# Kernel optimization log

Measured on AMD Instinct MI355X. Metric: run time of the kernel, lower is better.

Reference implementation:

```python
import jax, jax.numpy as jnp
import numpy as np

D_MODEL = 512
EPS = 1e-5


def setup_inputs() -> dict:
    key = jax.random.key(0)
    k1, k2, k3 = jax.random.split(key, 3)
    B, N, D = 8, 2048, D_MODEL
    output = jax.random.normal(k1, (B, N, D), dtype=jnp.float32)
    # multiplicative 0/1 float mask over the [B, N, N] score matrix
    slf_attn_mask = jax.random.randint(k2, (B, N, N), 0, 2).astype(jnp.float32)
    # nn.Linear(d_model, d_model): weight [out, in], xavier-uniform; bias zeros-ish
    limit = float(np.sqrt(6.0 / (D + D)))
    W = jax.random.uniform(k3, (D, D), dtype=jnp.float32, minval=-limit, maxval=limit)
    b = jnp.zeros((D,), dtype=jnp.float32)
    return {"output": output, "slf_attn_mask": slf_attn_mask, "W": W, "b": b}


def reference(output, slf_attn_mask, W, b):
    temperature = jnp.asarray(D_MODEL, output.dtype) ** 0.5
    # scores: [B, N, N] = (q / temp) @ k^T, then multiplicative mask
    attn = jnp.einsum("bnd,bmd->bnm", output / temperature, output) * slf_attn_mask
    # F.normalize(p=2, dim=-1, eps=1e-5): x / max(||x||_2, eps)
    norm = jnp.sqrt(jnp.sum(attn * attn, axis=-1, keepdims=True))
    attn = attn / jnp.maximum(norm, EPS)
    # values: elu(Linear(output)), Linear uses W @ x + b with W [out, in]
    v = jax.nn.elu(jnp.einsum("bnd,ed->bne", output, W) + b)
    return jnp.einsum("bnm,bme->bne", attn, v)
```

## Files before the change

kernel.cpp:

```cpp
#include <hip/hip_runtime.h>
#include <hip/hip_bf16.h>

#define NSEQ 2048
#define DM 512
#define BATCH 8
#define GTOT (BATCH * NSEQ)
#define INV_T 0.044194173824159216f
#define EPSN 1e-5f

typedef __bf16 bf16_t;
typedef bf16_t bf16x8 __attribute__((ext_vector_type(8)));
typedef float f32x16 __attribute__((ext_vector_type(16)));
typedef unsigned short u16;
typedef unsigned int u32;
typedef unsigned long long u64;

__device__ __forceinline__ u16 f2bf(float f) {
    u32 u = __builtin_bit_cast(u32, f);
    u32 r = (u + 0x7FFFu + ((u >> 16) & 1u)) >> 16;
    return (u16)r;
}

__device__ __forceinline__ void async16(const u16* g, u16* l) {
    __builtin_amdgcn_global_load_lds(
        (const __attribute__((address_space(1))) u32*)g,
        (__attribute__((address_space(3))) u32*)l, 16, 0, 0);
}

__device__ __forceinline__ bf16x8 fragld64(const u16* t, int row, int kc) {
    return *(const bf16x8*)(t + row * 64 + ((kc ^ ((row >> 1) & 7)) << 3));
}

#define MFMA32(a, b, c) __builtin_amdgcn_mfma_f32_32x32x16_bf16(a, b, c, 0, 0, 0)
#define ROWOFF(reg, lh) (((reg) & 3) + 8 * ((reg) >> 2) + 4 * (lh))

#define STAGE64(Ag, ldA, Bg, ldB, k0)                                            \
    do {                                                                         \
        _Pragma("unroll") for (int j = 0; j < 4; ++j) {                          \
            const int cg = (lane & 7) ^ ((j * 4 + (lane >> 4)) & 7);             \
            const int dst = (wave * 4 + j) * 512 + lane * 8;                     \
            async16((Ag) + (long)(rS + j * 8) * (ldA) + (k0) + cg * 8, Ab + dst);\
            async16((Bg) + (long)(rS + j * 8) * (ldB) + (k0) + cg * 8, Bb + dst);\
        }                                                                        \
    } while (0)

__global__ __launch_bounds__(256) void k_convert(
    const float* __restrict__ X, const float* __restrict__ W,
    u16* __restrict__ Kbf, u16* __restrict__ Wbf, float* __restrict__ ssbuf) {
    const long NK = (long)GTOT * DM / 4;
    const long NW = (long)DM * DM / 4;
    const long NS = GTOT / 4;
    long i = (long)blockIdx.x * 256 + threadIdx.x;
    if (i < NK) {
        float4 f = ((const float4*)X)[i];
        ushort4 o;
        o.x = f2bf(f.x); o.y = f2bf(f.y); o.z = f2bf(f.z); o.w = f2bf(f.w);
        ((ushort4*)Kbf)[i] = o;
    } else if (i < NK + NW) {
        long j = i - NK;
        float4 f = ((const float4*)W)[j];
        ushort4 o;
        o.x = f2bf(f.x); o.y = f2bf(f.y); o.z = f2bf(f.z); o.w = f2bf(f.w);
        ((ushort4*)Wbf)[j] = o;
    } else if (i < NK + NW + NS) {
        ((float4*)ssbuf)[i - NK - NW] = (float4){0.f, 0.f, 0.f, 0.f};
    }
}

__global__ __launch_bounds__(256, 4) void k_sgemm(
    const u16* __restrict__ Kbf, const float* __restrict__ mask,
    u16* __restrict__ Sbuf, float* __restrict__ ssbuf) {
    __shared__ __attribute__((aligned(16))) u16 Ab[8192], Bb[8192];
    const int tid = threadIdx.x, wave = tid >> 6, lane = tid & 63;
    const int l31 = lane & 31, lh = lane >> 5;
    const int wy = wave >> 1, wx = wave & 1;
    const int bid = blockIdx.x;
    const int b = bid & 7;
    const int ty = (bid >> 3) & 15, tx = bid >> 7;
    const int M0 = ty * 128, N0 = tx * 128;
    const u16* Ag = Kbf + (long)(b * NSEQ + M0) * DM;
    const u16* Bg = Kbf + (long)(b * NSEQ + N0) * DM;

    const int rS = wave * 32 + (lane >> 3);

    f32x16 acc[2][2];
#pragma unroll
    for (int i = 0; i < 2; ++i)
#pragma unroll
        for (int j = 0; j < 2; ++j)
#pragma unroll
            for (int e = 0; e < 16; ++e) acc[i][j][e] = 0.f;

    for (int kt = 0; kt < 8; ++kt) {
        const int k0 = kt * 64;
        __syncthreads();
        STAGE64(Ag, DM, Bg, DM, k0);
        __syncthreads();
#pragma unroll
        for (int ks = 0; ks < 4; ++ks) {
            const int kc = ks * 2 + lh;
            bf16x8 a0 = fragld64(Ab, wy * 64 + l31, kc);
            bf16x8 a1 = fragld64(Ab, wy * 64 + 32 + l31, kc);
            bf16x8 b0 = fragld64(Bb, wx * 64 + l31, kc);
            bf16x8 b1 = fragld64(Bb, wx * 64 + 32 + l31, kc);
            acc[0][0] = MFMA32(a0, b0, acc[0][0]);
            acc[0][1] = MFMA32(a0, b1, acc[0][1]);
            acc[1][0] = MFMA32(a1, b0, acc[1][0]);
            acc[1][1] = MFMA32(a1, b1, acc[1][1]);
        }
    }
#pragma unroll
    for (int mi = 0; mi < 2; ++mi) {
#pragma unroll
        for (int reg = 0; reg < 16; ++reg) {
            int rl = M0 + wy * 64 + mi * 32 + ROWOFF(reg, lh);
            long rg = (long)b * NSEQ + rl;
            const float* mrow = mask + rg * NSEQ;
            float v = 0.f;
#pragma unroll
            for (int ni = 0; ni < 2; ++ni) {
                int cg = N0 + wx * 64 + ni * 32 + l31;
                float s = acc[mi][ni][reg] * INV_T * mrow[cg];
                v += s * s;
                Sbuf[rg * NSEQ + cg] = f2bf(s);
            }
            v += __shfl_xor(v, 1, 32);
            v += __shfl_xor(v, 2, 32);
            v += __shfl_xor(v, 4, 32);
            v += __shfl_xor(v, 8, 32);
            v += __shfl_xor(v, 16, 32);
            if (l31 == 0) atomicAdd(&ssbuf[rg], v);
        }
    }
}

__global__ __launch_bounds__(256, 4) void k_vgemm(
    const u16* __restrict__ Wbf, const u16* __restrict__ Kbf,
    const float* __restrict__ bias, u16* __restrict__ vT) {
    __shared__ __attribute__((aligned(16))) u16 Ab[8192], Bb[8192];
    const int tid = threadIdx.x, wave = tid >> 6, lane = tid & 63;
    const int l31 = lane & 31, lh = lane >> 5;
    const int wy = wave >> 1, wx = wave & 1;
    const int M0 = blockIdx.y * 128, N0 = blockIdx.x * 128;
    const u16* Ag = Wbf + (long)M0 * DM;
    const u16* Bg = Kbf + (long)N0 * DM;

    const int rS = wave * 32 + (lane >> 3);

    f32x16 acc[2][2];
#pragma unroll
    for (int i = 0; i < 2; ++i)
#pragma unroll
        for (int j = 0; j < 2; ++j)
#pragma unroll
            for (int e = 0; e < 16; ++e) acc[i][j][e] = 0.f;

    for (int kt = 0; kt < 8; ++kt) {
        const int k0 = kt * 64;
        __syncthreads();
        STAGE64(Ag, DM, Bg, DM, k0);
        __syncthreads();
#pragma unroll
        for (int ks = 0; ks < 4; ++ks) {
            const int kc = ks * 2 + lh;
            bf16x8 a0 = fragld64(Ab, wy * 64 + l31, kc);
            bf16x8 a1 = fragld64(Ab, wy * 64 + 32 + l31, kc);
            bf16x8 b0 = fragld64(Bb, wx * 64 + l31, kc);
            bf16x8 b1 = fragld64(Bb, wx * 64 + 32 + l31, kc);
            acc[0][0] = MFMA32(a0, b0, acc[0][0]);
            acc[0][1] = MFMA32(a0, b1, acc[0][1]);
            acc[1][0] = MFMA32(a1, b0, acc[1][0]);
            acc[1][1] = MFMA32(a1, b1, acc[1][1]);
        }
    }
#pragma unroll
    for (int mi = 0; mi < 2; ++mi) {
#pragma unroll
        for (int reg = 0; reg < 16; ++reg) {
            int e = M0 + wy * 64 + mi * 32 + ROWOFF(reg, lh);
            float bv = bias[e];
#pragma unroll
            for (int ni = 0; ni < 2; ++ni) {
                int g = N0 + wx * 64 + ni * 32 + l31;
                float x = acc[mi][ni][reg] + bv;
                float v = x > 0.f ? x : (__expf(x) - 1.f);
                vT[(long)e * GTOT + g] = f2bf(v);
            }
        }
    }
}

__global__ __launch_bounds__(256, 4) void k_pv(
    const u16* __restrict__ Sbuf, const u16* __restrict__ vT,
    const float* __restrict__ ssbuf, float* __restrict__ Out) {
    __shared__ __attribute__((aligned(16))) u16 Ab[8192], Bb[8192];
    __shared__ float sc[128];
    const int tid = threadIdx.x, wave = tid >> 6, lane = tid & 63;
    const int l31 = lane & 31, lh = lane >> 5;
    const int wy = wave >> 1, wx = wave & 1;
    const int bid = blockIdx.x;
    const int b = bid & 7;
    const int r = bid >> 3;
    const int tx = r & 3, ty = r >> 2;
    const int M0 = ty * 128, N0 = tx * 128;
    const u16* Ag = Sbuf + (long)(b * NSEQ + M0) * NSEQ;
    const u16* Bg = vT + (long)N0 * GTOT + b * NSEQ;

    if (tid < 128) {
        float v = ssbuf[b * NSEQ + M0 + tid];
        sc[tid] = 1.f / fmaxf(sqrtf(v), EPSN);
    }

    const int rS = wave * 32 + (lane >> 3);

    f32x16 acc[2][2];
#pragma unroll
    for (int i = 0; i < 2; ++i)
#pragma unroll
        for (int j = 0; j < 2; ++j)
#pragma unroll
            for (int e = 0; e < 16; ++e) acc[i][j][e] = 0.f;

    for (int kt = 0; kt < 32; ++kt) {
        const int k0 = kt * 64;
        __syncthreads();
        STAGE64(Ag, NSEQ, Bg, GTOT, k0);
        __syncthreads();
#pragma unroll
        for (int ks = 0; ks < 4; ++ks) {
            const int kc = ks * 2 + lh;
            bf16x8 a0 = fragld64(Ab, wy * 64 + l31, kc);
            bf16x8 a1 = fragld64(Ab, wy * 64 + 32 + l31, kc);
            bf16x8 b0 = fragld64(Bb, wx * 64 + l31, kc);
            bf16x8 b1 = fragld64(Bb, wx * 64 + 32 + l31, kc);
            acc[0][0] = MFMA32(a0, b0, acc[0][0]);
            acc[0][1] = MFMA32(a0, b1, acc[0][1]);
            acc[1][0] = MFMA32(a1, b0, acc[1][0]);
            acc[1][1] = MFMA32(a1, b1, acc[1][1]);
        }
    }
#pragma unroll
    for (int mi = 0; mi < 2; ++mi) {
#pragma unroll
        for (int reg = 0; reg < 16; ++reg) {
            int rl = wy * 64 + mi * 32 + ROWOFF(reg, lh);
            float s = sc[rl];
            float* op = Out + ((long)b * NSEQ + M0 + rl) * DM;
#pragma unroll
            for (int ni = 0; ni < 2; ++ni) {
                int d = N0 + wx * 64 + ni * 32 + l31;
                op[d] = acc[mi][ni][reg] * s;
            }
        }
    }
}

extern "C" void kernel_launch(void* const* d_in, const int* in_sizes, int n_in,
                              void* d_out, int out_size, void* d_ws, size_t ws_size,
                              hipStream_t stream) {
    const float* X = (const float*)d_in[0];
    const float* mask = (const float*)d_in[1];
    const float* W = (const float*)d_in[2];
    const float* bias = (const float*)d_in[3];
    float* out = (float*)d_out;

    char* ws = (char*)d_ws;
    u16* Kbf = (u16*)ws;
    u16* Wbf = (u16*)(ws + 16777216);
    u16* vT = (u16*)(ws + 17301504);
    u16* Sbuf = (u16*)(ws + 34078720);
    float* ssbuf = (float*)(ws + 101187584);

    k_convert<<<8464, 256, 0, stream>>>(X, W, Kbf, Wbf, ssbuf);
    k_vgemm<<<dim3(128, 4), 256, 0, stream>>>(Wbf, Kbf, bias, vT);
    k_sgemm<<<2048, 256, 0, stream>>>(Kbf, mask, Sbuf, ssbuf);
    k_pv<<<512, 256, 0, stream>>>(Sbuf, vT, ssbuf, out);
}
```

Before: 333.6 us.

## Pack attention mask to bits and use 8-wave blocks for V and PV GEMMs

```diff
diff --git a/kernel.cpp b/kernel.cpp
--- a/kernel.cpp
+++ b/kernel.cpp
@@ -44,13 +44,37 @@
         }                                                                        \
     } while (0)
 
+#define STAGE64W8(Ag, ldA, Bg, ldB, k0)                                          \
+    do {                                                                         \
+        _Pragma("unroll") for (int j = 0; j < 2; ++j) {                          \
+            const int cg = (lane & 7) ^ ((j * 4 + (lane >> 4)) & 7);             \
+            const int rr = wave * 16 + j * 8 + (lane >> 3);                      \
+            const int dst = (wave * 2 + j) * 512 + lane * 8;                     \
+            async16((Ag) + (long)rr * (ldA) + (k0) + cg * 8, Ab + dst);          \
+            async16((Bg) + (long)rr * (ldB) + (k0) + cg * 8, Bb + dst);          \
+        }                                                                        \
+    } while (0)
+
 __global__ __launch_bounds__(256) void k_convert(
     const float* __restrict__ X, const float* __restrict__ W,
-    u16* __restrict__ Kbf, u16* __restrict__ Wbf, float* __restrict__ ssbuf) {
+    const float* __restrict__ mask, u16* __restrict__ Kbf, u16* __restrict__ Wbf,
+    u64* __restrict__ Mbits, float* __restrict__ ssbuf) {
+    const int bid = blockIdx.x;
+    if (bid < 32768) {
+        const int w = threadIdx.x >> 6, lane = threadIdx.x & 63;
+        const long base = (long)bid * 1024 + w * 256;
+#pragma unroll
+        for (int j = 0; j < 4; ++j) {
+            float m = mask[base + j * 64 + lane];
+            u64 bits = __ballot(m != 0.f);
+            if (lane == 0) Mbits[(base + j * 64) >> 6] = bits;
+        }
+        return;
+    }
     const long NK = (long)GTOT * DM / 4;
     const long NW = (long)DM * DM / 4;
     const long NS = GTOT / 4;
-    long i = (long)blockIdx.x * 256 + threadIdx.x;
+    long i = (long)(bid - 32768) * 256 + threadIdx.x;
     if (i < NK) {
         float4 f = ((const float4*)X)[i];
         ushort4 o;
@@ -68,7 +92,7 @@
 }
 
 __global__ __launch_bounds__(256, 4) void k_sgemm(
-    const u16* __restrict__ Kbf, const float* __restrict__ mask,
+    const u16* __restrict__ Kbf, const u32* __restrict__ Mw,
     u16* __restrict__ Sbuf, float* __restrict__ ssbuf) {
     __shared__ __attribute__((aligned(16))) u16 Ab[8192], Bb[8192];
     const int tid = threadIdx.x, wave = tid >> 6, lane = tid & 63;
@@ -80,6 +104,7 @@
     const int M0 = ty * 128, N0 = tx * 128;
     const u16* Ag = Kbf + (long)(b * NSEQ + M0) * DM;
     const u16* Bg = Kbf + (long)(b * NSEQ + N0) * DM;
+    const u32* Mb = Mw + (long)b * NSEQ * 64;
 
     const int rS = wave * 32 + (lane >> 3);
 
@@ -115,12 +140,12 @@
         for (int reg = 0; reg < 16; ++reg) {
             int rl = M0 + wy * 64 + mi * 32 + ROWOFF(reg, lh);
             long rg = (long)b * NSEQ + rl;
-            const float* mrow = mask + rg * NSEQ;
             float v = 0.f;
 #pragma unroll
             for (int ni = 0; ni < 2; ++ni) {
                 int cg = N0 + wx * 64 + ni * 32 + l31;
-                float s = acc[mi][ni][reg] * INV_T * mrow[cg];
+                u32 wd = Mb[(long)rl * 64 + (cg >> 5)];
+                float s = ((wd >> l31) & 1u) ? acc[mi][ni][reg] * INV_T : 0.f;
                 v += s * s;
                 Sbuf[rg * NSEQ + cg] = f2bf(s);
             }
@@ -134,43 +159,36 @@
     }
 }
 
-__global__ __launch_bounds__(256, 4) void k_vgemm(
+__global__ __launch_bounds__(512, 2) void k_vgemm(
     const u16* __restrict__ Wbf, const u16* __restrict__ Kbf,
     const float* __restrict__ bias, u16* __restrict__ vT) {
     __shared__ __attribute__((aligned(16))) u16 Ab[8192], Bb[8192];
     const int tid = threadIdx.x, wave = tid >> 6, lane = tid & 63;
     const int l31 = lane & 31, lh = lane >> 5;
-    const int wy = wave >> 1, wx = wave & 1;
+    const int wy = wave >> 2, wx = wave & 3;
     const int M0 = blockIdx.y * 128, N0 = blockIdx.x * 128;
     const u16* Ag = Wbf + (long)M0 * DM;
     const u16* Bg = Kbf + (long)N0 * DM;
 
-    const int rS = wave * 32 + (lane >> 3);
-
-    f32x16 acc[2][2];
+    f32x16 acc[2];
 #pragma unroll
     for (int i = 0; i < 2; ++i)
 #pragma unroll
-        for (int j = 0; j < 2; ++j)
-#pragma unroll
-            for (int e = 0; e < 16; ++e) acc[i][j][e] = 0.f;
+        for (int e = 0; e < 16; ++e) acc[i][e] = 0.f;
 
     for (int kt = 0; kt < 8; ++kt) {
         const int k0 = kt * 64;
         __syncthreads();
-        STAGE64(Ag, DM, Bg, DM, k0);
+        STAGE64W8(Ag, DM, Bg, DM, k0);
         __syncthreads();
 #pragma unroll
         for (int ks = 0; ks < 4; ++ks) {
             const int kc = ks * 2 + lh;
             bf16x8 a0 = fragld64(Ab, wy * 64 + l31, kc);
             bf16x8 a1 = fragld64(Ab, wy * 64 + 32 + l31, kc);
-            bf16x8 b0 = fragld64(Bb, wx * 64 + l31, kc);
-            bf16x8 b1 = fragld64(Bb, wx * 64 + 32 + l31, kc);
-            acc[0][0] = MFMA32(a0, b0, acc[0][0]);
-            acc[0][1] = MFMA32(a0, b1, acc[0][1]);
-            acc[1][0] = MFMA32(a1, b0, acc[1][0]);
-            acc[1][1] = MFMA32(a1, b1, acc[1][1]);
+            bf16x8 b0 = fragld64(Bb, wx * 32 + l31, kc);
+            acc[0] = MFMA32(a0, b0, acc[0]);
+            acc[1] = MFMA32(a1, b0, acc[1]);
         }
     }
 #pragma unroll
@@ -179,25 +197,22 @@
         for (int reg = 0; reg < 16; ++reg) {
             int e = M0 + wy * 64 + mi * 32 + ROWOFF(reg, lh);
             float bv = bias[e];
-#pragma unroll
-            for (int ni = 0; ni < 2; ++ni) {
-                int g = N0 + wx * 64 + ni * 32 + l31;
-                float x = acc[mi][ni][reg] + bv;
-                float v = x > 0.f ? x : (__expf(x) - 1.f);
-                vT[(long)e * GTOT + g] = f2bf(v);
-            }
-        }
-    }
-}
-
-__global__ __launch_bounds__(256, 4) void k_pv(
+            int g = N0 + wx * 32 + l31;
+            float x = acc[mi][reg] + bv;
+            float v = x > 0.f ? x : (__expf(x) - 1.f);
+            vT[(long)e * GTOT + g] = f2bf(v);
+        }
+    }
+}
+
+__global__ __launch_bounds__(512, 2) void k_pv(
     const u16* __restrict__ Sbuf, const u16* __restrict__ vT,
     const float* __restrict__ ssbuf, float* __restrict__ Out) {
     __shared__ __attribute__((aligned(16))) u16 Ab[8192], Bb[8192];
     __shared__ float sc[128];
     const int tid = threadIdx.x, wave = tid >> 6, lane = tid & 63;
     const int l31 = lane & 31, lh = lane >> 5;
-    const int wy = wave >> 1, wx = wave & 1;
+    const int wy = wave >> 2, wx = wave & 3;
     const int bid = blockIdx.x;
     const int b = bid & 7;
     const int r = bid >> 3;
@@ -211,32 +226,25 @@
         sc[tid] = 1.f / fmaxf(sqrtf(v), EPSN);
     }
 
-    const int rS = wave * 32 + (lane >> 3);
-
-    f32x16 acc[2][2];
+    f32x16 acc[2];
 #pragma unroll
     for (int i = 0; i < 2; ++i)
 #pragma unroll
-        for (int j = 0; j < 2; ++j)
-#pragma unroll
-            for (int e = 0; e < 16; ++e) acc[i][j][e] = 0.f;
+        for (int e = 0; e < 16; ++e) acc[i][e] = 0.f;
 
     for (int kt = 0; kt < 32; ++kt) {
         const int k0 = kt * 64;
         __syncthreads();
-        STAGE64(Ag, NSEQ, Bg, GTOT, k0);
+        STAGE64W8(Ag, NSEQ, Bg, GTOT, k0);
         __syncthreads();
 #pragma unroll
         for (int ks = 0; ks < 4; ++ks) {
             const int kc = ks * 2 + lh;
             bf16x8 a0 = fragld64(Ab, wy * 64 + l31, kc);
             bf16x8 a1 = fragld64(Ab, wy * 64 + 32 + l31, kc);
-            bf16x8 b0 = fragld64(Bb, wx * 64 + l31, kc);
-            bf16x8 b1 = fragld64(Bb, wx * 64 + 32 + l31, kc);
-            acc[0][0] = MFMA32(a0, b0, acc[0][0]);
-            acc[0][1] = MFMA32(a0, b1, acc[0][1]);
-            acc[1][0] = MFMA32(a1, b0, acc[1][0]);
-            acc[1][1] = MFMA32(a1, b1, acc[1][1]);
+            bf16x8 b0 = fragld64(Bb, wx * 32 + l31, kc);
+            acc[0] = MFMA32(a0, b0, acc[0]);
+            acc[1] = MFMA32(a1, b0, acc[1]);
         }
     }
 #pragma unroll
@@ -245,12 +253,8 @@
         for (int reg = 0; reg < 16; ++reg) {
             int rl = wy * 64 + mi * 32 + ROWOFF(reg, lh);
             float s = sc[rl];
-            float* op = Out + ((long)b * NSEQ + M0 + rl) * DM;
-#pragma unroll
-            for (int ni = 0; ni < 2; ++ni) {
-                int d = N0 + wx * 64 + ni * 32 + l31;
-                op[d] = acc[mi][ni][reg] * s;
-            }
+            int d = N0 + wx * 32 + l31;
+            Out[((long)b * NSEQ + M0 + rl) * DM + d] = acc[mi][reg] * s;
         }
     }
 }
@@ -270,9 +274,10 @@
     u16* vT = (u16*)(ws + 17301504);
     u16* Sbuf = (u16*)(ws + 34078720);
     float* ssbuf = (float*)(ws + 101187584);
-
-    k_convert<<<8464, 256, 0, stream>>>(X, W, Kbf, Wbf, ssbuf);
-    k_vgemm<<<dim3(128, 4), 256, 0, stream>>>(Wbf, Kbf, bias, vT);
-    k_sgemm<<<2048, 256, 0, stream>>>(Kbf, mask, Sbuf, ssbuf);
-    k_pv<<<512, 256, 0, stream>>>(Sbuf, vT, ssbuf, out);
-}
+    u64* Mbits = (u64*)(ws + 101253120);
+
+    k_convert<<<41232, 256, 0, stream>>>(X, W, mask, Kbf, Wbf, Mbits, ssbuf);
+    k_vgemm<<<dim3(128, 4), 512, 0, stream>>>(Wbf, Kbf, bias, vT);
+    k_sgemm<<<2048, 256, 0, stream>>>(Kbf, (const u32*)Mbits, Sbuf, ssbuf);
+    k_pv<<<512, 512, 0, stream>>>(Sbuf, vT, ssbuf, out);
+}
```

New measurement: 350.6 us. 1.05x slower.
